# Kernel tuning notes

Measured on AMD Instinct MI355X. Metric: run time of the kernel, lower is better.

Reference implementation:

```python
import jax, jax.numpy as jnp
import numpy as np

POS_DIM = 3
CAPACITY = 262144  # 2**18 hash-table slots per level
NR_LEVELS = 24
NR_FEAT = 2
N_POINTS = 524288
HASH_MUL = 2531011  # permutohedral-lattice hash multiplier (uint32 wraparound)


def _permuto_encode(positions, lattice_values, random_shift, anneal_window, scale_per_level):
    # positions: [N,d]  lattice_values: [L,C,F]  random_shift: [L,d]
    # anneal_window: [L]  scale_per_level: [L]
    N, d = positions.shape
    L, C, F = lattice_values.shape
    dp1 = d + 1
    dim = jnp.arange(d, dtype=positions.dtype)
    # per-level, per-axis scale: s_l / sqrt((i+1)(i+2))
    scale_factor = scale_per_level[:, None] / jnp.sqrt((dim + 1.0) * (dim + 2.0))  # [L,d]
    cf = (positions[None, :, :] + random_shift[:, None, :]) * scale_factor[:, None, :]  # [L,N,d]
    # elevate onto the hyperplane sum(x)=0 in R^{d+1}:
    # elevated[0]=sum(cf); elevated[i]=sum(cf[i:]) - i*cf[i-1]
    S = jnp.cumsum(cf[..., ::-1], axis=-1)[..., ::-1]            # suffix sums S[i]=sum cf[i:]
    S_next = jnp.concatenate([S[..., 1:], jnp.zeros_like(S[..., :1])], axis=-1)
    i_arr = jnp.arange(1, dp1, dtype=positions.dtype)
    elevated = jnp.concatenate([S[..., :1], S_next - i_arr * cf], axis=-1)  # [L,N,d+1]
    # nearest remainder-0 lattice point (round each coord to multiple of d+1)
    v = elevated / dp1
    up = jnp.ceil(v) * dp1
    down = jnp.floor(v) * dp1
    rem0 = jnp.where(up - elevated < elevated - down, up, down)  # [L,N,d+1]
    sum_val = jnp.round(jnp.sum(rem0, axis=-1) / dp1).astype(jnp.int32)  # [L,N]
    # rank: for i<j, if diff_i < diff_j then rank_i++ else rank_j++
    diff = elevated - rem0
    di = diff[..., :, None]
    dj = diff[..., None, :]
    ii = jnp.arange(dp1)[:, None]
    jj = jnp.arange(dp1)[None, :]
    rank = jnp.sum(jnp.where(jj > ii, dj > di, (jj < ii) & (dj >= di)), axis=-1).astype(jnp.int32)
    rank = rank + sum_val[..., None]
    under = rank < 0
    over = rank > d
    rank = rank + dp1 * under.astype(jnp.int32) - dp1 * over.astype(jnp.int32)
    rem0 = rem0 + dp1 * (under.astype(rem0.dtype) - over.astype(rem0.dtype))
    # barycentric weights: bary[d-rank_i] += delta_i; bary[d+1-rank_i] -= delta_i; bary[0] += 1 + bary[d+1]
    delta = (elevated - rem0) / dp1  # [L,N,d+1]
    t = d - rank
    bary = []
    for k in range(dp1 + 1):
        mk = (t == k).astype(delta.dtype) - (t == k - 1).astype(delta.dtype)
        bary.append(jnp.sum(delta * mk, axis=-1))  # [L,N]
    bary[0] = bary[0] + 1.0 + bary[dp1]
    # hash the d+1 simplex vertices; key[i] = rem0[i] + r - (d+1)*[rank[i] > d-r]
    rem0i = jnp.round(rem0).astype(jnp.int32)
    r = jnp.arange(dp1, dtype=jnp.int32)  # remainder axis -> simplex vertex
    h = jnp.zeros((L, N, dp1), dtype=jnp.uint32)
    for i in range(d):  # tiny structural loop over pos_dim
        key_i = rem0i[..., i:i + 1] + r - dp1 * (rank[..., i:i + 1] > d - r).astype(jnp.int32)
        h = (h + key_i.astype(jnp.uint32)) * jnp.uint32(HASH_MUL)
    ix = (h % jnp.uint32(C)).astype(jnp.int32)  # [L,N,d+1]
    # gather the d+1 vertex feature vectors per level and blend barycentrically
    gather = jax.vmap(lambda table, idx: table[idx])  # vmap over levels
    out = jnp.zeros((L, N, F), dtype=lattice_values.dtype)
    for rr in range(dp1):  # tiny structural loop over simplex vertices
        out = out + bary[rr][..., None] * gather(lattice_values, ix[..., rr])
    out = out * anneal_window[:, None, None]
    # kernel outputs [L,F,N] -> permute(2,0,1).reshape(N, L*F)
    return jnp.transpose(out, (1, 0, 2)).reshape(N, L * F)


def setup_inputs() -> dict:
    key = jax.random.key(0)
    k1, k2, k3 = jax.random.split(key, 3)
    positions = jax.random.uniform(k1, (N_POINTS, POS_DIM), dtype=jnp.float32)
    lattice_values = jax.random.normal(k2, (NR_LEVELS, CAPACITY, NR_FEAT), dtype=jnp.float32) * 1e-5
    random_shift = jax.random.normal(k3, (NR_LEVELS, POS_DIM), dtype=jnp.float32) * 10.0
    anneal_window = jnp.ones((NR_LEVELS,), dtype=jnp.float32)
    scale_per_level = jnp.asarray(np.geomspace(16.0, 2048.0, NR_LEVELS), dtype=jnp.float32)
    return {"positions": positions, "lattice_values": lattice_values,
            "random_shift": random_shift, "anneal_window": anneal_window,
            "scale_per_level": scale_per_level}


def reference(positions, lattice_values, random_shift, anneal_window, scale_per_level):
    return _permuto_encode(positions, lattice_values, random_shift, anneal_window, scale_per_level)
```

## Files before the change

kernel.cpp:

```cpp
#include <hip/hip_runtime.h>
#include <cstdint>

#define NPOINTS 524288
#define NLEV 24
#define CAP 262144
#define NFEAT 2
#define HASHMUL 2531011u
#define BLOCKS_PER_LEVEL (NPOINTS / 256)

template <bool USE_WS>
__global__ __launch_bounds__(256) void permuto_kernel(
    const float* __restrict__ pos,
    const float* __restrict__ lattice,
    const float* __restrict__ shift,
    const float* __restrict__ anneal,
    const float* __restrict__ scale,
    float2* __restrict__ ws,
    float* __restrict__ out)
{
    const int bid  = blockIdx.x;
    const int xcd  = bid & 7;
    const int slot = bid >> 3;
    const int l    = xcd + 8 * (slot >> 11);
    const int nb   = slot & (BLOCKS_PER_LEVEL - 1);
    const int n    = (nb << 8) + threadIdx.x;

    const float sc  = scale[l];
    const float sf0 = sc / sqrtf(2.0f);
    const float sf1 = sc / sqrtf(6.0f);
    const float sf2 = sc / sqrtf(12.0f);
    const float sh0 = shift[l*3+0];
    const float sh1 = shift[l*3+1];
    const float sh2 = shift[l*3+2];
    const float an  = anneal[l];

    const float p0 = pos[n*3+0];
    const float p1 = pos[n*3+1];
    const float p2 = pos[n*3+2];

    const float cf0 = (p0 + sh0) * sf0;
    const float cf1 = (p1 + sh1) * sf1;
    const float cf2 = (p2 + sh2) * sf2;

    const float S2 = cf2;
    const float S1 = cf2 + cf1;
    const float S0 = S1 + cf0;

    float E[4];
    E[0] = S0;
    E[1] = S1 - 1.0f*cf0;
    E[2] = S2 - 2.0f*cf1;
    E[3] = 0.0f - 3.0f*cf2;

    float rem0[4];
    float sumrem = 0.0f;
    #pragma unroll
    for (int i = 0; i < 4; ++i) {
        float v  = E[i] * 0.25f;
        float up = ceilf(v)  * 4.0f;
        float dn = floorf(v) * 4.0f;
        rem0[i] = (up - E[i] < E[i] - dn) ? up : dn;
        sumrem += rem0[i];
    }
    const int sum_val = (int)rintf(sumrem * 0.25f);

    float diff[4];
    #pragma unroll
    for (int i = 0; i < 4; ++i) diff[i] = E[i] - rem0[i];

    int rank[4];
    #pragma unroll
    for (int i = 0; i < 4; ++i) {
        int rk = 0;
        #pragma unroll
        for (int j = 0; j < 4; ++j) {
            if (j > i)      rk += (diff[j] >  diff[i]) ? 1 : 0;
            else if (j < i) rk += (diff[j] >= diff[i]) ? 1 : 0;
        }
        rk += sum_val;
        if (rk < 0)      { rk += 4; rem0[i] += 4.0f; }
        else if (rk > 3) { rk -= 4; rem0[i] -= 4.0f; }
        rank[i] = rk;
    }

    float delta[4];
    #pragma unroll
    for (int i = 0; i < 4; ++i) delta[i] = (E[i] - rem0[i]) * 0.25f;

    float b[5];
    #pragma unroll
    for (int k = 0; k < 5; ++k) {
        float acc = 0.0f;
        #pragma unroll
        for (int i = 0; i < 4; ++i) {
            int ti = 3 - rank[i];
            float m = ((ti == k) ? 1.0f : 0.0f) - ((ti == (k-1)) ? 1.0f : 0.0f);
            acc += delta[i] * m;
        }
        b[k] = acc;
    }
    b[0] += 1.0f + b[4];

    int rem0i[4];
    #pragma unroll
    for (int i = 0; i < 4; ++i) rem0i[i] = (int)rintf(rem0[i]);

    const float* tbl = lattice + (size_t)l * (CAP * NFEAT);
    float o0 = 0.0f, o1 = 0.0f;
    #pragma unroll
    for (int r = 0; r < 4; ++r) {
        uint32_t h = 0u;
        #pragma unroll
        for (int i = 0; i < 3; ++i) {
            int key = rem0i[i] + r - 4 * ((rank[i] > 3 - r) ? 1 : 0);
            h = (h + (uint32_t)key) * HASHMUL;
        }
        uint32_t ix = h & (uint32_t)(CAP - 1);
        const float2 val = *reinterpret_cast<const float2*>(tbl + (size_t)ix * 2);
        o0 += b[r] * val.x;
        o1 += b[r] * val.y;
    }

    float2 res;
    res.x = o0 * an;
    res.y = o1 * an;
    if (USE_WS) {
        ws[(size_t)l * NPOINTS + n] = res;
    } else {
        *reinterpret_cast<float2*>(out + (size_t)n * (NLEV*NFEAT) + l*NFEAT) = res;
    }
}

__global__ __launch_bounds__(256) void transpose_kernel(
    const float* __restrict__ ws,
    float* __restrict__ out)
{
    __shared__ float lds[128 * 49];
    const int t  = threadIdx.x;
    const int n0 = blockIdx.x * 128;

    #pragma unroll
    for (int l = 0; l < NLEV; ++l) {
        const float v = ws[(size_t)l * (NPOINTS*2) + (size_t)n0 * 2 + t];
        const int p = t >> 1;
        const int f = t & 1;
        lds[p * 49 + l * 2 + f] = v;
    }
    __syncthreads();

    const size_t obase = (size_t)n0 * 48;
    #pragma unroll
    for (int it = 0; it < 24; ++it) {
        const int flat = it * 256 + t;
        const int p = flat / 48;
        const int c = flat - p * 48;
        out[obase + flat] = lds[p * 49 + c];
    }
}

extern "C" void kernel_launch(void* const* d_in, const int* in_sizes, int n_in,
                              void* d_out, int out_size, void* d_ws, size_t ws_size,
                              hipStream_t stream) {
    const float* pos     = (const float*)d_in[0];
    const float* lattice = (const float*)d_in[1];
    const float* shift   = (const float*)d_in[2];
    const float* anneal  = (const float*)d_in[3];
    const float* scale   = (const float*)d_in[4];
    float* out = (float*)d_out;

    const int grid = NLEV * BLOCKS_PER_LEVEL;
    const size_t ws_needed = (size_t)NLEV * NPOINTS * 2 * sizeof(float);

    if (ws_size >= ws_needed) {
        float2* ws = (float2*)d_ws;
        permuto_kernel<true><<<grid, 256, 0, stream>>>(
            pos, lattice, shift, anneal, scale, ws, out);
        transpose_kernel<<<NPOINTS / 128, 256, 0, stream>>>(
            (const float*)d_ws, out);
    } else {
        permuto_kernel<false><<<grid, 256, 0, stream>>>(
            pos, lattice, shift, anneal, scale, nullptr, out);
    }
}
```

Before: 246.9 us.

## Process two points per thread with LDS-staged positions and batched gathers

Each thread now handles two points per level, so the 8 hash-table gathers are issued together to raise memory-level parallelism. Positions are staged through shared memory with coalesced loads instead of strided per-thread loads. Workspace writes become nontemporal stores, and launch bounds request 6 blocks per CU. The cost is more registers per thread and half as many blocks in the grid.

Result: no change. 251.8 us (+2.0%).

```diff
diff --git a/kernel.cpp b/kernel.cpp
--- a/kernel.cpp
+++ b/kernel.cpp
@@ -4,12 +4,98 @@
 #define NPOINTS 524288
 #define NLEV 24
 #define CAP 262144
-#define NFEAT 2
 #define HASHMUL 2531011u
-#define BLOCKS_PER_LEVEL (NPOINTS / 256)
+#define PTS_PER_BLOCK 512
+#define BLOCKS_PER_LEVEL (NPOINTS / PTS_PER_BLOCK)
+
+__device__ __forceinline__ void prep_point(
+    const float p0, const float p1, const float p2,
+    const float sf0, const float sf1, const float sf2,
+    const float sh0, const float sh1, const float sh2,
+    uint32_t* __restrict__ ix, float* __restrict__ w)
+{
+    const float cf0 = (p0 + sh0) * sf0;
+    const float cf1 = (p1 + sh1) * sf1;
+    const float cf2 = (p2 + sh2) * sf2;
+
+    const float S2 = cf2;
+    const float S1 = cf2 + cf1;
+    const float S0 = S1 + cf0;
+
+    float E[4];
+    E[0] = S0;
+    E[1] = S1 - 1.0f*cf0;
+    E[2] = S2 - 2.0f*cf1;
+    E[3] = 0.0f - 3.0f*cf2;
+
+    float rem0[4];
+    float sumrem = 0.0f;
+    #pragma unroll
+    for (int i = 0; i < 4; ++i) {
+        float v  = E[i] * 0.25f;
+        float up = ceilf(v)  * 4.0f;
+        float dn = floorf(v) * 4.0f;
+        rem0[i] = (up - E[i] < E[i] - dn) ? up : dn;
+        sumrem += rem0[i];
+    }
+    const int sum_val = (int)rintf(sumrem * 0.25f);
+
+    float diff[4];
+    #pragma unroll
+    for (int i = 0; i < 4; ++i) diff[i] = E[i] - rem0[i];
+
+    int rank[4];
+    #pragma unroll
+    for (int i = 0; i < 4; ++i) {
+        int rk = 0;
+        #pragma unroll
+        for (int j = 0; j < 4; ++j) {
+            if (j > i)      rk += (diff[j] >  diff[i]) ? 1 : 0;
+            else if (j < i) rk += (diff[j] >= diff[i]) ? 1 : 0;
+        }
+        rk += sum_val;
+        if (rk < 0)      { rk += 4; rem0[i] += 4.0f; }
+        else if (rk > 3) { rk -= 4; rem0[i] -= 4.0f; }
+        rank[i] = rk;
+    }
+
+    float delta[4];
+    #pragma unroll
+    for (int i = 0; i < 4; ++i) delta[i] = (E[i] - rem0[i]) * 0.25f;
+
+    float b[5];
+    #pragma unroll
+    for (int k = 0; k < 5; ++k) {
+        float acc = 0.0f;
+        #pragma unroll
+        for (int i = 0; i < 4; ++i) {
+            int ti = 3 - rank[i];
+            float m = ((ti == k) ? 1.0f : 0.0f) - ((ti == (k-1)) ? 1.0f : 0.0f);
+            acc += delta[i] * m;
+        }
+        b[k] = acc;
+    }
+    b[0] += 1.0f + b[4];
+
+    int rem0i[4];
+    #pragma unroll
+    for (int i = 0; i < 4; ++i) rem0i[i] = (int)rintf(rem0[i]);
+
+    #pragma unroll
+    for (int r = 0; r < 4; ++r) {
+        uint32_t h = 0u;
+        #pragma unroll
+        for (int i = 0; i < 3; ++i) {
+            int key = rem0i[i] + r - 4 * ((rank[i] > 3 - r) ? 1 : 0);
+            h = (h + (uint32_t)key) * HASHMUL;
+        }
+        ix[r] = h & (uint32_t)(CAP - 1);
+        w[r]  = b[r];
+    }
+}
 
 template <bool USE_WS>
-__global__ __launch_bounds__(256) void permuto_kernel(
+__global__ __launch_bounds__(256, 6) void permuto_kernel(
     const float* __restrict__ pos,
     const float* __restrict__ lattice,
     const float* __restrict__ shift,
@@ -18,12 +104,22 @@
     float2* __restrict__ ws,
     float* __restrict__ out)
 {
+    __shared__ float s_pos[PTS_PER_BLOCK * 3];
+
+    const int t    = threadIdx.x;
     const int bid  = blockIdx.x;
     const int xcd  = bid & 7;
     const int slot = bid >> 3;
-    const int l    = xcd + 8 * (slot >> 11);
+    const int l    = xcd + 8 * (slot >> 10);
     const int nb   = slot & (BLOCKS_PER_LEVEL - 1);
-    const int n    = (nb << 8) + threadIdx.x;
+    const int pbase = nb * PTS_PER_BLOCK;
+
+    {
+        const float* src = pos + (size_t)pbase * 3;
+        #pragma unroll
+        for (int k = 0; k < 6; ++k)
+            s_pos[k * 256 + t] = src[k * 256 + t];
+    }
 
     const float sc  = scale[l];
     const float sf0 = sc / sqrtf(2.0f);
@@ -34,100 +130,46 @@
     const float sh2 = shift[l*3+2];
     const float an  = anneal[l];
 
-    const float p0 = pos[n*3+0];
-    const float p1 = pos[n*3+1];
-    const float p2 = pos[n*3+2];
-
-    const float cf0 = (p0 + sh0) * sf0;
-    const float cf1 = (p1 + sh1) * sf1;
-    const float cf2 = (p2 + sh2) * sf2;
-
-    const float S2 = cf2;
-    const float S1 = cf2 + cf1;
-    const float S0 = S1 + cf0;
-
-    float E[4];
-    E[0] = S0;
-    E[1] = S1 - 1.0f*cf0;
-    E[2] = S2 - 2.0f*cf1;
-    E[3] = 0.0f - 3.0f*cf2;
-
-    float rem0[4];
-    float sumrem = 0.0f;
-    #pragma unroll
-    for (int i = 0; i < 4; ++i) {
-        float v  = E[i] * 0.25f;
-        float up = ceilf(v)  * 4.0f;
-        float dn = floorf(v) * 4.0f;
-        rem0[i] = (up - E[i] < E[i] - dn) ? up : dn;
-        sumrem += rem0[i];
-    }
-    const int sum_val = (int)rintf(sumrem * 0.25f);
-
-    float diff[4];
-    #pragma unroll
-    for (int i = 0; i < 4; ++i) diff[i] = E[i] - rem0[i];
-
-    int rank[4];
-    #pragma unroll
-    for (int i = 0; i < 4; ++i) {
-        int rk = 0;
-        #pragma unroll
-        for (int j = 0; j < 4; ++j) {
-            if (j > i)      rk += (diff[j] >  diff[i]) ? 1 : 0;
-            else if (j < i) rk += (diff[j] >= diff[i]) ? 1 : 0;
-        }
-        rk += sum_val;
-        if (rk < 0)      { rk += 4; rem0[i] += 4.0f; }
-        else if (rk > 3) { rk -= 4; rem0[i] -= 4.0f; }
-        rank[i] = rk;
-    }
-
-    float delta[4];
-    #pragma unroll
-    for (int i = 0; i < 4; ++i) delta[i] = (E[i] - rem0[i]) * 0.25f;
-
-    float b[5];
-    #pragma unroll
-    for (int k = 0; k < 5; ++k) {
-        float acc = 0.0f;
-        #pragma unroll
-        for (int i = 0; i < 4; ++i) {
-            int ti = 3 - rank[i];
-            float m = ((ti == k) ? 1.0f : 0.0f) - ((ti == (k-1)) ? 1.0f : 0.0f);
-            acc += delta[i] * m;
-        }
-        b[k] = acc;
-    }
-    b[0] += 1.0f + b[4];
-
-    int rem0i[4];
-    #pragma unroll
-    for (int i = 0; i < 4; ++i) rem0i[i] = (int)rintf(rem0[i]);
-
-    const float* tbl = lattice + (size_t)l * (CAP * NFEAT);
-    float o0 = 0.0f, o1 = 0.0f;
+    __syncthreads();
+
+    const float a0 = s_pos[3*t+0], a1 = s_pos[3*t+1], a2 = s_pos[3*t+2];
+    const float b0 = s_pos[3*(t+256)+0], b1 = s_pos[3*(t+256)+1], b2 = s_pos[3*(t+256)+2];
+
+    uint32_t ixA[4], ixB[4];
+    float    wA[4],  wB[4];
+    prep_point(a0, a1, a2, sf0, sf1, sf2, sh0, sh1, sh2, ixA, wA);
+    prep_point(b0, b1, b2, sf0, sf1, sf2, sh0, sh1, sh2, ixB, wB);
+
+    const float2* __restrict__ tbl =
+        reinterpret_cast<const float2*>(lattice) + (size_t)l * CAP;
+
+    float2 vA[4], vB[4];
+    #pragma unroll
+    for (int r = 0; r < 4; ++r) vA[r] = tbl[ixA[r]];
+    #pragma unroll
+    for (int r = 0; r < 4; ++r) vB[r] = tbl[ixB[r]];
+
+    float oA0 = 0.f, oA1 = 0.f, oB0 = 0.f, oB1 = 0.f;
     #pragma unroll
     for (int r = 0; r < 4; ++r) {
-        uint32_t h = 0u;
-        #pragma unroll
-        for (int i = 0; i < 3; ++i) {
-            int key = rem0i[i] + r - 4 * ((rank[i] > 3 - r) ? 1 : 0);
-            h = (h + (uint32_t)key) * HASHMUL;
-        }
-        uint32_t ix = h & (uint32_t)(CAP - 1);
-        const float2 val = *reinterpret_cast<const float2*>(tbl + (size_t)ix * 2);
-        o0 += b[r] * val.x;
-        o1 += b[r] * val.y;
-    }
-
-    float2 res;
-    res.x = o0 * an;
-    res.y = o1 * an;
+        oA0 += wA[r] * vA[r].x;  oA1 += wA[r] * vA[r].y;
+        oB0 += wB[r] * vB[r].x;  oB1 += wB[r] * vB[r].y;
+    }
+
+    float2 resA, resB;
+    resA.x = oA0 * an;  resA.y = oA1 * an;
+    resB.x = oB0 * an;  resB.y = oB1 * an;
+
     if (USE_WS) {
-        ws[(size_t)l * NPOINTS + n] = res;
+        float2* pA = ws + (size_t)l * NPOINTS + pbase + t;
+        float2* pB = pA + 256;
+        __builtin_nontemporal_store(resA.x, &pA->x);
+        __builtin_nontemporal_store(resA.y, &pA->y);
+        __builtin_nontemporal_store(resB.x, &pB->x);
+        __builtin_nontemporal_store(resB.y, &pB->y);
     } else {
-        *reinterpret_cast<float2*>(out + (size_t)n * (NLEV*NFEAT) + l*NFEAT) = res;
+        *reinterpret_cast<float2*>(out + (size_t)(pbase + t) * (NLEV*2) + l*2) = resA;
+        *reinterpret_cast<float2*>(out + (size_t)(pbase + 256 + t) * (NLEV*2) + l*2) = resB;
     }
 }
 
```
